# Kernel optimization log

Measured on AMD Instinct MI355X. Metric: run time of the kernel, lower is better.

The kernel has to match this reference:

```python
import jax, jax.numpy as jnp
import numpy as np

D = 768

def setup_inputs() -> dict:
    key = jax.random.key(0)
    ks = jax.random.split(key, 8)
    s = 1.0 / np.sqrt(D)
    return {
        "sentence_rep": jax.random.normal(ks[0], (32, 512, D), dtype=jnp.float32),
        "comment_rep": jax.random.normal(ks[1], (32, 2048, D), dtype=jnp.float32),
        "Wq": jax.random.uniform(ks[2], (D, D), jnp.float32, -s, s),
        "bq": jax.random.uniform(ks[3], (D,), jnp.float32, -s, s),
        "Wk": jax.random.uniform(ks[4], (D, D), jnp.float32, -s, s),
        "bk": jax.random.uniform(ks[5], (D,), jnp.float32, -s, s),
        "Wv": jax.random.uniform(ks[6], (D, D), jnp.float32, -s, s),
        "bv": jax.random.uniform(ks[7], (D,), jnp.float32, -s, s),
    }

def reference(sentence_rep, comment_rep, Wq, bq, Wk, bk, Wv, bv):
    # query: [B, Lq, D]; key/value: [B, Lk, D]
    query = jnp.einsum('bqd,ed->bqe', sentence_rep, Wq) + bq
    key_ = jnp.einsum('bkd,ed->bke', comment_rep, Wk) + bk
    value = jnp.einsum('bkd,ed->bke', comment_rep, Wv) + bv
    # sum_q (Q K^T) == (sum_q Q) K^T  -> avoids the [B, Lq, Lk] score matrix
    q_sum = query.sum(axis=1)                       # [B, D]
    scores = jnp.einsum('bd,bkd->bk', q_sum, key_)  # [B, Lk]
    alpha = jax.nn.softmax(scores, axis=-1)         # [B, Lk]
    return jnp.einsum('bk,bkd->bd', alpha, value)   # [B, D]
```

## Files before the change

### kernel.cpp

```cpp
#include <hip/hip_runtime.h>
#include <math.h>

#define B 32
#define LQ 512
#define LK 2048
#define D 768
#define D4 192
#define NC 32

__global__ __launch_bounds__(192) void k_sum_sent(const float4* __restrict__ sent,
                                                  float* __restrict__ s_sum) {
    int b = blockIdx.x, qc = blockIdx.y;
    int d4 = threadIdx.x;
    const float4* p = sent + ((size_t)b * LQ + (size_t)qc * 16) * D4 + d4;
    float4 acc = make_float4(0.f, 0.f, 0.f, 0.f);
#pragma unroll
    for (int q = 0; q < 16; ++q) {
        float4 v = p[(size_t)q * D4];
        acc.x += v.x; acc.y += v.y; acc.z += v.z; acc.w += v.w;
    }
    float* dst = s_sum + b * D + d4 * 4;
    atomicAdd(dst + 0, acc.x);
    atomicAdd(dst + 1, acc.y);
    atomicAdd(dst + 2, acc.z);
    atomicAdd(dst + 3, acc.w);
}

__global__ __launch_bounds__(256) void k_rowdot(const float4* __restrict__ x4,
                                                const float4* __restrict__ W4,
                                                const float* __restrict__ bias,
                                                float bias_scale,
                                                float* __restrict__ y) {
    int w = blockIdx.x * 4 + (threadIdx.x >> 6);
    int lane = threadIdx.x & 63;
    int b = w / D, e = w % D;
    const float4* xr = x4 + (size_t)b * D4;
    const float4* wr = W4 + (size_t)e * D4;
    float acc = 0.f;
#pragma unroll
    for (int i = 0; i < 3; ++i) {
        int idx = lane + i * 64;
        float4 a = xr[idx], q = wr[idx];
        acc += a.x * q.x + a.y * q.y + a.z * q.z + a.w * q.w;
    }
#pragma unroll
    for (int off = 32; off; off >>= 1) acc += __shfl_down(acc, off, 64);
    if (lane == 0) y[w] = acc + bias_scale * bias[e];
}

__global__ __launch_bounds__(256) void k_qsum_Wk(const float* __restrict__ q_sum,
                                                 const float* __restrict__ Wk,
                                                 float* __restrict__ wk) {
    int b = blockIdx.x;
    int d = blockIdx.y * 256 + threadIdx.x;
    const float* qs = q_sum + b * D;
    float acc = 0.f;
#pragma unroll 8
    for (int e = 0; e < D; ++e)
        acc += qs[e] * Wk[(size_t)e * D + d];
    wk[b * D + d] = acc;
}

__global__ __launch_bounds__(256) void k_attn(const float4* __restrict__ com4,
                                              const float* __restrict__ wk,
                                              float* __restrict__ pv,
                                              float* __restrict__ pm,
                                              float* __restrict__ pl) {
    __shared__ float sm[4], sl[4];
    __shared__ float sacc[4][D];
    int b = blockIdx.x, chunk = blockIdx.y;
    int tid = threadIdx.x, lane = tid & 63, w = tid >> 6;

    const float4* q4 = (const float4*)(wk + (size_t)b * D);
    float4 q0 = q4[lane], q1 = q4[lane + 64], q2 = q4[lane + 128];

    int row0 = chunk * 64 + w * 16;
    const float4* base = com4 + ((size_t)b * LK + row0) * D4;

    float m = -INFINITY, l = 0.f;
    float4 A0 = make_float4(0.f, 0.f, 0.f, 0.f);
    float4 A1 = make_float4(0.f, 0.f, 0.f, 0.f);
    float4 A2 = make_float4(0.f, 0.f, 0.f, 0.f);

    for (int r = 0; r < 16; ++r) {
        float4 c0 = base[(size_t)r * D4 + lane];
        float4 c1 = base[(size_t)r * D4 + lane + 64];
        float4 c2 = base[(size_t)r * D4 + lane + 128];
        float s = c0.x * q0.x + c0.y * q0.y + c0.z * q0.z + c0.w * q0.w
                + c1.x * q1.x + c1.y * q1.y + c1.z * q1.z + c1.w * q1.w
                + c2.x * q2.x + c2.y * q2.y + c2.z * q2.z + c2.w * q2.w;
#pragma unroll
        for (int off = 32; off; off >>= 1) s += __shfl_xor(s, off, 64);
        if (s <= m) {
            float p = __expf(s - m);
            l += p;
            A0.x += p * c0.x; A0.y += p * c0.y; A0.z += p * c0.z; A0.w += p * c0.w;
            A1.x += p * c1.x; A1.y += p * c1.y; A1.z += p * c1.z; A1.w += p * c1.w;
            A2.x += p * c2.x; A2.y += p * c2.y; A2.z += p * c2.z; A2.w += p * c2.w;
        } else {
            float f = __expf(m - s);
            l = l * f + 1.f;
            A0.x = A0.x * f + c0.x; A0.y = A0.y * f + c0.y; A0.z = A0.z * f + c0.z; A0.w = A0.w * f + c0.w;
            A1.x = A1.x * f + c1.x; A1.y = A1.y * f + c1.y; A1.z = A1.z * f + c1.z; A1.w = A1.w * f + c1.w;
            A2.x = A2.x * f + c2.x; A2.y = A2.y * f + c2.y; A2.z = A2.z * f + c2.z; A2.w = A2.w * f + c2.w;
            m = s;
        }
    }

    if (lane == 0) { sm[w] = m; sl[w] = l; }
    float4* sa = (float4*)sacc[w];
    sa[lane] = A0; sa[lane + 64] = A1; sa[lane + 128] = A2;
    __syncthreads();

    float M = fmaxf(fmaxf(sm[0], sm[1]), fmaxf(sm[2], sm[3]));
    float e0 = __expf(sm[0] - M), e1 = __expf(sm[1] - M);
    float e2 = __expf(sm[2] - M), e3 = __expf(sm[3] - M);
    float L = sl[0] * e0 + sl[1] * e1 + sl[2] * e2 + sl[3] * e3;

    int col = tid * 3;
    float* dst = pv + ((size_t)b * NC + chunk) * D;
#pragma unroll
    for (int j = 0; j < 3; ++j) {
        int c = col + j;
        dst[c] = sacc[0][c] * e0 + sacc[1][c] * e1 + sacc[2][c] * e2 + sacc[3][c] * e3;
    }
    if (tid == 0) { pm[b * NC + chunk] = M; pl[b * NC + chunk] = L; }
}

__global__ __launch_bounds__(256) void k_merge(const float* __restrict__ pv,
                                               const float* __restrict__ pm,
                                               const float* __restrict__ pl,
                                               float* __restrict__ ctx) {
    __shared__ float spm[NC], spl[NC];
    int b = blockIdx.x, tid = threadIdx.x;
    if (tid < NC) { spm[tid] = pm[b * NC + tid]; spl[tid] = pl[b * NC + tid]; }
    __syncthreads();
    float M = -INFINITY;
#pragma unroll
    for (int c = 0; c < NC; ++c) M = fmaxf(M, spm[c]);
    float L = 0.f;
#pragma unroll
    for (int c = 0; c < NC; ++c) L += spl[c] * __expf(spm[c] - M);
    float inv = 1.f / L;
    int col = tid * 3;
    float o0 = 0.f, o1 = 0.f, o2 = 0.f;
    for (int c = 0; c < NC; ++c) {
        float e = __expf(spm[c] - M);
        const float* p = pv + ((size_t)b * NC + c) * D + col;
        o0 += e * p[0]; o1 += e * p[1]; o2 += e * p[2];
    }
    ctx[b * D + col] = o0 * inv;
    ctx[b * D + col + 1] = o1 * inv;
    ctx[b * D + col + 2] = o2 * inv;
}

extern "C" void kernel_launch(void* const* d_in, const int* in_sizes, int n_in,
                              void* d_out, int out_size, void* d_ws, size_t ws_size,
                              hipStream_t stream) {
    const float* sent = (const float*)d_in[0];
    const float* com  = (const float*)d_in[1];
    const float* Wq   = (const float*)d_in[2];
    const float* bq   = (const float*)d_in[3];
    const float* Wk   = (const float*)d_in[4];
    const float* Wv   = (const float*)d_in[6];
    const float* bv   = (const float*)d_in[7];
    float* out = (float*)d_out;

    float* ws = (float*)d_ws;
    float* s_sum = ws;
    float* q_sum = ws + 24576;
    float* wk    = ws + 49152;
    float* ctx   = ws + 73728;
    float* pm    = ws + 98304;
    float* pl    = ws + 99328;
    float* pv    = ws + 100352;

    hipMemsetAsync(s_sum, 0, 24576 * sizeof(float), stream);

    k_sum_sent<<<dim3(B, 32), 192, 0, stream>>>((const float4*)sent, s_sum);

    k_rowdot<<<6144, 256, 0, stream>>>((const float4*)s_sum, (const float4*)Wq,
                                       bq, (float)LQ, q_sum);

    k_qsum_Wk<<<dim3(B, 3), 256, 0, stream>>>(q_sum, Wk, wk);

    k_attn<<<dim3(B, NC), 256, 0, stream>>>((const float4*)com, wk, pv, pm, pl);

    k_merge<<<B, 256, 0, stream>>>(pv, pm, pl, ctx);

    k_rowdot<<<6144, 256, 0, stream>>>((const float4*)ctx, (const float4*)Wv,
                                       bv, 1.0f, out);
}
```

Measured before the change: 399.3 us.

## Replace atomic sentence sum with two-pass reduction and double the attention chunks

The sentence-sum kernel now writes per-chunk partials to workspace, and a second kernel reduces them. This removes the float atomics and the memset, at the cost of an extra launch and a 3 MB partial buffer. The attention kernel doubles the chunk count (NC 64, 8 rows per wave) for more blocks in flight, and software-prefetches the next row into registers. The price is more partial results for the merge kernel to combine.

```diff
diff --git a/kernel.cpp b/kernel.cpp
--- a/kernel.cpp
+++ b/kernel.cpp
@@ -6,10 +6,11 @@
 #define LK 2048
 #define D 768
 #define D4 192
-#define NC 32
-
-__global__ __launch_bounds__(192) void k_sum_sent(const float4* __restrict__ sent,
-                                                  float* __restrict__ s_sum) {
+#define NC 64
+#define SC 32
+
+__global__ __launch_bounds__(192) void k_sum_part(const float4* __restrict__ sent,
+                                                  float4* __restrict__ part4) {
     int b = blockIdx.x, qc = blockIdx.y;
     int d4 = threadIdx.x;
     const float4* p = sent + ((size_t)b * LQ + (size_t)qc * 16) * D4 + d4;
@@ -19,11 +20,18 @@
         float4 v = p[(size_t)q * D4];
         acc.x += v.x; acc.y += v.y; acc.z += v.z; acc.w += v.w;
     }
-    float* dst = s_sum + b * D + d4 * 4;
-    atomicAdd(dst + 0, acc.x);
-    atomicAdd(dst + 1, acc.y);
-    atomicAdd(dst + 2, acc.z);
-    atomicAdd(dst + 3, acc.w);
+    part4[((size_t)b * SC + qc) * D4 + d4] = acc;
+}
+
+__global__ __launch_bounds__(256) void k_sum_reduce(const float* __restrict__ part,
+                                                    float* __restrict__ s_sum) {
+    int b = blockIdx.x;
+    int d = blockIdx.y * 256 + threadIdx.x;
+    float acc = 0.f;
+#pragma unroll 8
+    for (int c = 0; c < SC; ++c)
+        acc += part[((size_t)b * SC + c) * D + d];
+    s_sum[b * D + d] = acc;
 }
 
 __global__ __launch_bounds__(256) void k_rowdot(const float4* __restrict__ x4,
@@ -74,7 +82,7 @@
     const float4* q4 = (const float4*)(wk + (size_t)b * D);
     float4 q0 = q4[lane], q1 = q4[lane + 64], q2 = q4[lane + 128];
 
-    int row0 = chunk * 64 + w * 16;
+    int row0 = chunk * 32 + w * 8;
     const float4* base = com4 + ((size_t)b * LK + row0) * D4;
 
     float m = -INFINITY, l = 0.f;
@@ -82,10 +90,14 @@
     float4 A1 = make_float4(0.f, 0.f, 0.f, 0.f);
     float4 A2 = make_float4(0.f, 0.f, 0.f, 0.f);
 
-    for (int r = 0; r < 16; ++r) {
-        float4 c0 = base[(size_t)r * D4 + lane];
-        float4 c1 = base[(size_t)r * D4 + lane + 64];
-        float4 c2 = base[(size_t)r * D4 + lane + 128];
+    float4 c0 = base[lane], c1 = base[lane + 64], c2 = base[lane + 128];
+#pragma unroll
+    for (int r = 0; r < 8; ++r) {
+        float4 n0, n1, n2;
+        if (r < 7) {
+            const float4* nb = base + (size_t)(r + 1) * D4;
+            n0 = nb[lane]; n1 = nb[lane + 64]; n2 = nb[lane + 128];
+        }
         float s = c0.x * q0.x + c0.y * q0.y + c0.z * q0.z + c0.w * q0.w
                 + c1.x * q1.x + c1.y * q1.y + c1.z * q1.z + c1.w * q1.w
                 + c2.x * q2.x + c2.y * q2.y + c2.z * q2.z + c2.w * q2.w;
@@ -105,6 +117,7 @@
             A2.x = A2.x * f + c2.x; A2.y = A2.y * f + c2.y; A2.z = A2.z * f + c2.z; A2.w = A2.w * f + c2.w;
             m = s;
         }
+        c0 = n0; c1 = n1; c2 = n2;
     }
 
     if (lane == 0) { sm[w] = m; sl[w] = l; }
@@ -167,17 +180,17 @@
     float* out = (float*)d_out;
 
     float* ws = (float*)d_ws;
-    float* s_sum = ws;
-    float* q_sum = ws + 24576;
-    float* wk    = ws + 49152;
-    float* ctx   = ws + 73728;
-    float* pm    = ws + 98304;
-    float* pl    = ws + 99328;
-    float* pv    = ws + 100352;
-
-    hipMemsetAsync(s_sum, 0, 24576 * sizeof(float), stream);
-
-    k_sum_sent<<<dim3(B, 32), 192, 0, stream>>>((const float4*)sent, s_sum);
+    float* part  = ws;
+    float* s_sum = ws + 786432;
+    float* q_sum = ws + 811008;
+    float* wk    = ws + 835584;
+    float* ctx   = ws + 860160;
+    float* pm    = ws + 884736;
+    float* pl    = ws + 886784;
+    float* pv    = ws + 888832;
+
+    k_sum_part<<<dim3(B, SC), 192, 0, stream>>>((const float4*)sent, (float4*)part);
+    k_sum_reduce<<<dim3(B, 3), 256, 0, stream>>>(part, s_sum);
 
     k_rowdot<<<6144, 256, 0, stream>>>((const float4*)s_sum, (const float4*)Wq,
                                        bq, (float)LQ, q_sum);
```

New measurement: 402.0 us. Within noise of the previous version (+0.7%).
